# Performance work log

Measured on AMD Instinct MI355X. Metric: run time of the kernel, lower is better.

Reference implementation:

```python
import jax, jax.numpy as jnp
import numpy as np
import math

NUM_HIDDEN = 512

def setup_inputs() -> dict:
    key = jax.random.key(0)
    k1, k2 = jax.random.split(key)
    a = jax.random.normal(k1, (8, 2048, NUM_HIDDEN), dtype=jnp.float32)
    b = jax.random.normal(k2, (8, 2048, NUM_HIDDEN), dtype=jnp.float32)
    return {"a": a, "b": b}

def reference(a, b):
    # simi_matrix: [B, La, Lb] = a @ b^T / sqrt(H)
    scale = 1.0 / math.sqrt(NUM_HIDDEN)
    simi = jnp.einsum('bld,bmd->blm', a, b) * scale
    norm_weight = jax.nn.softmax(simi, axis=2)
    # up_1: [B, La, H] = attn @ b + residual a
    up_1 = jnp.einsum('blm,bmd->bld', norm_weight, b) + a
    return up_1
```

## Files before the change

kernel.cpp:

```cpp
#include <hip/hip_runtime.h>
#include <hip/hip_bf16.h>

#define D 512
#define NSEQ 2048
#define NB 8
#define QBLK 64
#define KVBLK 64
#define NTHREADS 512
#define NT (NSEQ / KVBLK)
#define ROWE 2112
#define BUFE (16 * ROWE)
#define SROWP 68
#define PROWP 72
#define CROWP 68
#define DEFER_THR 8.0f

typedef __attribute__((ext_vector_type(8))) short bf16x8;
typedef __attribute__((ext_vector_type(4))) float f32x4;
typedef __attribute__((ext_vector_type(4))) unsigned short u16x4;
typedef __attribute__((ext_vector_type(4))) int i32x4;

static __device__ __forceinline__ unsigned short f2b(float f) {
  unsigned u = __builtin_bit_cast(unsigned, f);
  return (unsigned short)((u + 0x7FFFu + ((u >> 16) & 1u)) >> 16);
}

__global__ __launch_bounds__(256) void conv_dual(const float* __restrict__ in,
                                                 unsigned short* __restrict__ b16,
                                                 unsigned short* __restrict__ bT) {
  __shared__ unsigned short tile[64 * CROWP];
  const int bid = blockIdx.x;
  const int batch = bid >> 8;
  const int rem = bid & 255;
  const int kvt = rem >> 3;
  const int dt  = rem & 7;
  const int t = threadIdx.x;
  const int r = t >> 2;
  const int c = (t & 3) * 16;

  const float* src = in + ((size_t)batch * NSEQ + kvt * 64 + r) * D + dt * 64 + c;
  unsigned short* o16 = b16 + ((size_t)batch * NSEQ + kvt * 64 + r) * D + dt * 64 + c;

  float4 v0 = *reinterpret_cast<const float4*>(src);
  float4 v1 = *reinterpret_cast<const float4*>(src + 4);
  float4 v2 = *reinterpret_cast<const float4*>(src + 8);
  float4 v3 = *reinterpret_cast<const float4*>(src + 12);
  bf16x8 h0, h1;
  h0[0] = (short)f2b(v0.x); h0[1] = (short)f2b(v0.y);
  h0[2] = (short)f2b(v0.z); h0[3] = (short)f2b(v0.w);
  h0[4] = (short)f2b(v1.x); h0[5] = (short)f2b(v1.y);
  h0[6] = (short)f2b(v1.z); h0[7] = (short)f2b(v1.w);
  h1[0] = (short)f2b(v2.x); h1[1] = (short)f2b(v2.y);
  h1[2] = (short)f2b(v2.z); h1[3] = (short)f2b(v2.w);
  h1[4] = (short)f2b(v3.x); h1[5] = (short)f2b(v3.y);
  h1[6] = (short)f2b(v3.z); h1[7] = (short)f2b(v3.w);
  *reinterpret_cast<bf16x8*>(o16)     = h0;
  *reinterpret_cast<bf16x8*>(o16 + 8) = h1;
  #pragma unroll
  for (int i = 0; i < 4; ++i) {
    u16x4 w;
    w[0] = (unsigned short)((i < 2 ? h0 : h1)[(i & 1) * 4 + 0]);
    w[1] = (unsigned short)((i < 2 ? h0 : h1)[(i & 1) * 4 + 1]);
    w[2] = (unsigned short)((i < 2 ? h0 : h1)[(i & 1) * 4 + 2]);
    w[3] = (unsigned short)((i < 2 ? h0 : h1)[(i & 1) * 4 + 3]);
    *reinterpret_cast<u16x4*>(&tile[r * CROWP + c + i * 4]) = w;
  }
  __syncthreads();

  const int w  = t >> 6;
  const int dr = t & 63;
  unsigned short* oT = bT + (size_t)batch * D * NSEQ
                          + (size_t)(dt * 64 + dr) * NSEQ + kvt * 64 + w * 16;
  unsigned short g[16];
  #pragma unroll
  for (int i = 0; i < 16; ++i)
    g[i] = tile[(w * 16 + i) * CROWP + dr];
  bf16x8 p0, p1;
  #pragma unroll
  for (int i = 0; i < 8; ++i) { p0[i] = (short)g[i]; p1[i] = (short)g[8 + i]; }
  *reinterpret_cast<bf16x8*>(oT)     = p0;
  *reinterpret_cast<bf16x8*>(oT + 8) = p1;
}

__global__ __launch_bounds__(NTHREADS, 1)
void attn_v17(const float* __restrict__ A, const unsigned short* __restrict__ B16,
              const unsigned short* __restrict__ T16, float* __restrict__ Out) {
  __shared__ __align__(16) unsigned short Bs[BUFE];
  __shared__ __align__(16) unsigned short Bt[D * KVBLK];
  __shared__ __align__(16) float Ss[QBLK * SROWP];
  __shared__ __align__(16) unsigned short Ps[QBLK * PROWP];
  __shared__ float mS[QBLK];
  __shared__ float lS[QBLK];
  __shared__ float aS[QBLK];
  __shared__ __align__(16) int flagS[8];

  const int tid  = threadIdx.x;
  const int wid  = tid >> 6;
  const int lane = tid & 63;
  const int l16  = lane & 15;
  const int g4   = lane >> 4;

  const int batch = blockIdx.x & 7;
  const int qt    = blockIdx.x >> 3;
  const int qbase = qt * QBLK;

  const float*          Ab = A   + (size_t)batch * NSEQ * D;
  const unsigned short* Kb = B16 + (size_t)batch * NSEQ * D;
  const unsigned short* Tb = T16 + (size_t)batch * D * NSEQ;
  float*                Ob = Out + (size_t)batch * NSEQ * D;

  const float scale = 0.04419417382415922f;

  const int qi = wid >> 1;
  const int kp = wid & 1;

  const float* Arow = Ab + (size_t)(qbase + qi * 16 + l16) * D;
  bf16x8 qf[16];
  #pragma unroll
  for (int ks = 0; ks < 16; ++ks) {
    int d0 = ks * 32 + g4 * 8;
    float4 v0 = *reinterpret_cast<const float4*>(Arow + d0);
    float4 v1 = *reinterpret_cast<const float4*>(Arow + d0 + 4);
    bf16x8 f;
    f[0] = (short)f2b(v0.x * scale); f[1] = (short)f2b(v0.y * scale);
    f[2] = (short)f2b(v0.z * scale); f[3] = (short)f2b(v0.w * scale);
    f[4] = (short)f2b(v1.x * scale); f[5] = (short)f2b(v1.y * scale);
    f[6] = (short)f2b(v1.z * scale); f[7] = (short)f2b(v1.w * scale);
    qf[ks] = f;
  }
  if (tid < QBLK) { mS[tid] = -1e30f; lS[tid] = 0.f; }

  f32x4 acc[4][4];
  #pragma unroll
  for (int mi = 0; mi < 4; ++mi)
    #pragma unroll
    for (int ni = 0; ni < 4; ++ni)
      acc[mi][ni] = (f32x4){0.f, 0.f, 0.f, 0.f};

  #pragma unroll
  for (int c = 0; c < 8; ++c) {
    int id = wid * 8 + c;
    int g = id >> 2, q = id & 3;
    const unsigned short* src = Kb
        + (size_t)(g * 4 + ((lane >> 1) & 3)) * D
        + q * 128 + (lane >> 3) * 16 + (lane & 1) * 8;
    unsigned short* dst = &Bs[g * ROWE + q * 512];
    __builtin_amdgcn_global_load_lds(
        (const __attribute__((address_space(1))) void*)src,
        (__attribute__((address_space(3))) void*)dst, 16, 0, 0);
  }
  #pragma unroll
  for (int c = 0; c < 8; ++c) {
    int drow = wid * 64 + c * 8 + (lane >> 3);
    int chunk = (lane & 7) ^ ((lane >> 3) & 7);
    const unsigned short* src = Tb + (size_t)drow * NSEQ + chunk * 8;
    unsigned short* dst = (unsigned short*)&Bt[(wid * 64 + c * 8) * KVBLK];
    __builtin_amdgcn_global_load_lds(
        (const __attribute__((address_space(1))) void*)src,
        (__attribute__((address_space(3))) void*)dst, 16, 0, 0);
  }
  asm volatile("s_waitcnt vmcnt(0)" ::: "memory");
  asm volatile("s_waitcnt lgkmcnt(0)" ::: "memory");
  __builtin_amdgcn_s_barrier();

  const int bbase0 = ((kp * 2) * 4 + (l16 >> 2)) * ROWE + (l16 & 3) * 16 + (g4 & 1) * 8;
  const int bbase1 = bbase0 + 4 * ROWE;

  for (int kt = 0; kt < NT; ++kt) {
    {
      f32x4 s0 = {0.f, 0.f, 0.f, 0.f};
      f32x4 s1 = {0.f, 0.f, 0.f, 0.f};
      __builtin_amdgcn_s_setprio(1);
      #pragma unroll
      for (int ks = 0; ks < 16; ++ks) {
        const int ro = (ks * 2 + (g4 >> 1)) * 64;
        const bf16x8 b0 = *reinterpret_cast<const bf16x8*>(&Bs[bbase0 + ro]);
        const bf16x8 b1 = *reinterpret_cast<const bf16x8*>(&Bs[bbase1 + ro]);
        s0 = __builtin_amdgcn_mfma_f32_16x16x32_bf16(qf[ks], b0, s0, 0, 0, 0);
        s1 = __builtin_amdgcn_mfma_f32_16x16x32_bf16(qf[ks], b1, s1, 0, 0, 0);
      }
      __builtin_amdgcn_s_setprio(0);
      #pragma unroll
      for (int r = 0; r < 4; ++r) {
        Ss[(qi * 16 + g4 * 4 + r) * SROWP + (kp * 2) * 16 + l16]     = s0[r];
        Ss[(qi * 16 + g4 * 4 + r) * SROWP + (kp * 2 + 1) * 16 + l16] = s1[r];
      }
    }
    asm volatile("s_waitcnt lgkmcnt(0)" ::: "memory");
    __builtin_amdgcn_s_barrier();

    if (kt + 1 < NT) {
      const unsigned short* Kt = Kb + (size_t)(kt + 1) * KVBLK * D;
      #pragma unroll
      for (int c = 0; c < 8; ++c) {
        int id = wid * 8 + c;
        int g = id >> 2, q = id & 3;
        const unsigned short* src = Kt
            + (size_t)(g * 4 + ((lane >> 1) & 3)) * D
            + q * 128 + (lane >> 3) * 16 + (lane & 1) * 8;
        unsigned short* dst = &Bs[g * ROWE + q * 512];
        __builtin_amdgcn_global_load_lds(
            (const __attribute__((address_space(1))) void*)src,
            (__attribute__((address_space(3))) void*)dst, 16, 0, 0);
      }
    }

    {
      int row = wid * 8 + (lane >> 3);
      int c   = lane & 7;
      float sv[8];
      #pragma unroll
      for (int j = 0; j < 8; ++j)
        sv[j] = Ss[row * SROWP + c + 8 * j];
      float m01 = fmaxf(sv[0], sv[1]), m23 = fmaxf(sv[2], sv[3]);
      float m45 = fmaxf(sv[4], sv[5]), m67 = fmaxf(sv[6], sv[7]);
      float mloc = fmaxf(fmaxf(m01, m23), fmaxf(m45, m67));
      #pragma unroll
      for (int off = 1; off < 8; off <<= 1)
        mloc = fmaxf(mloc, __shfl_xor(mloc, off));
      float mold = mS[row];
      int defer = (mloc <= mold + DEFER_THR) ? 1 : 0;
      float mnew = defer ? mold : mloc;
      float al = defer ? 1.0f : __expf(mold - mnew);
      float psum = 0.f;
      #pragma unroll
      for (int j = 0; j < 8; ++j) {
        float p = __expf(sv[j] - mnew);
        psum += p;
        Ps[row * PROWP + c + 8 * j] = f2b(p);
      }
      #pragma unroll
      for (int off = 1; off < 8; off <<= 1)
        psum += __shfl_xor(psum, off);
      int wave_defer = __all(defer);
      if (c == 0) {
        mS[row] = mnew;
        lS[row] = lS[row] * al + psum;
        aS[row] = al;
      }
      if (lane == 0) flagS[wid] = wave_defer;
    }
    asm volatile("s_waitcnt lgkmcnt(0)" ::: "memory");
    if (kt + 1 < NT) {
      asm volatile("s_waitcnt vmcnt(8)" ::: "memory");
    } else {
      asm volatile("s_waitcnt vmcnt(0)" ::: "memory");
    }
    __builtin_amdgcn_s_barrier();

    {
      i32x4 f0 = *reinterpret_cast<const i32x4*>(&flagS[0]);
      i32x4 f1 = *reinterpret_cast<const i32x4*>(&flagS[4]);
      int allskip = f0[0] & f0[1] & f0[2] & f0[3] & f1[0] & f1[1] & f1[2] & f1[3];
      if (!allskip) {
        #pragma unroll
        for (int mi = 0; mi < 4; ++mi) {
          float a = aS[mi * 16 + l16];
          #pragma unroll
          for (int ni = 0; ni < 4; ++ni)
            #pragma unroll
            for (int r = 0; r < 4; ++r)
              acc[mi][ni][r] *= a;
        }
      }

      const char* Bc = (const char*)&Bt[0];
      __builtin_amdgcn_s_setprio(1);
      #pragma unroll
      for (int ks = 0; ks < 2; ++ks) {
        bf16x8 pf[4];
        #pragma unroll
        for (int mi = 0; mi < 4; ++mi)
          pf[mi] = *reinterpret_cast<const bf16x8*>(
              &Ps[(mi * 16 + l16) * PROWP + ks * 32 + g4 * 8]);
        #pragma unroll
        for (int ni = 0; ni < 4; ++ni) {
          int row = wid * 64 + ni * 16 + l16;
          int swz = (ks * 4 + g4) ^ (l16 & 7);
          const bf16x8 vf = *reinterpret_cast<const bf16x8*>(Bc + row * 128 + swz * 16);
          #pragma unroll
          for (int mi = 0; mi < 4; ++mi)
            acc[mi][ni] = __builtin_amdgcn_mfma_f32_16x16x32_bf16(vf, pf[mi], acc[mi][ni], 0, 0, 0);
        }
      }
      __builtin_amdgcn_s_setprio(0);
    }
    asm volatile("s_waitcnt lgkmcnt(0)" ::: "memory");

    if (kt + 1 < NT) {
      #pragma unroll
      for (int c = 0; c < 8; ++c) {
        int drow = wid * 64 + c * 8 + (lane >> 3);
        int chunk = (lane & 7) ^ ((lane >> 3) & 7);
        const unsigned short* src = Tb + (size_t)drow * NSEQ + (kt + 1) * KVBLK + chunk * 8;
        unsigned short* dst = (unsigned short*)&Bt[(wid * 64 + c * 8) * KVBLK];
        __builtin_amdgcn_global_load_lds(
            (const __attribute__((address_space(1))) void*)src,
            (__attribute__((address_space(3))) void*)dst, 16, 0, 0);
      }
      asm volatile("s_waitcnt vmcnt(8)" ::: "memory");
    }
    __builtin_amdgcn_s_barrier();
  }

  #pragma unroll
  for (int mi = 0; mi < 4; ++mi) {
    float rl = 1.0f / lS[mi * 16 + l16];
    int q = qbase + mi * 16 + l16;
    #pragma unroll
    for (int ni = 0; ni < 4; ++ni) {
      int d = wid * 64 + ni * 16 + g4 * 4;
      const float4 av = *reinterpret_cast<const float4*>(Ab + (size_t)q * D + d);
      float4 o;
      o.x = acc[mi][ni][0] * rl + av.x;
      o.y = acc[mi][ni][1] * rl + av.y;
      o.z = acc[mi][ni][2] * rl + av.z;
      o.w = acc[mi][ni][3] * rl + av.w;
      *reinterpret_cast<float4*>(Ob + (size_t)q * D + d) = o;
    }
  }
}

#define FQBLK 32
#define FSROWP (64 + 4)
#define FPROWP (64 + 8)
__global__ __launch_bounds__(NTHREADS, 2)
void attn_fb(const float* __restrict__ A, const float* __restrict__ B32,
             float* __restrict__ Out) {
  __shared__ __align__(16) unsigned short Bs[BUFE];
  __shared__ float Ss[FQBLK * FSROWP];
  __shared__ unsigned short Ps[FQBLK * FPROWP];
  __shared__ float mS[FQBLK];
  __shared__ float lS[FQBLK];
  __shared__ float aS[FQBLK];

  const int tid  = threadIdx.x;
  const int wid  = tid >> 6;
  const int lane = tid & 63;
  const int l16  = lane & 15;
  const int g4   = lane >> 4;

  const int batch = blockIdx.x & 7;
  const int qt    = blockIdx.x >> 3;
  const int qbase = qt * FQBLK;

  const float* Ab   = A   + (size_t)batch * NSEQ * D;
  const float* Bb32 = B32 + (size_t)batch * NSEQ * D;
  float*       Ob   = Out + (size_t)batch * NSEQ * D;

  const float scale = 0.04419417382415922f;

  const int qi = wid >> 2;
  const int ki = wid & 3;

  const float* Arow = Ab + (size_t)(qbase + qi * 16 + l16) * D;
  bf16x8 qf[16];
  #pragma unroll
  for (int ks = 0; ks < 16; ++ks) {
    int d0 = ks * 32 + g4 * 8;
    float4 v0 = *reinterpret_cast<const float4*>(Arow + d0);
    float4 v1 = *reinterpret_cast<const float4*>(Arow + d0 + 4);
    bf16x8 f;
    f[0] = (short)f2b(v0.x * scale); f[1] = (short)f2b(v0.y * scale);
    f[2] = (short)f2b(v0.z * scale); f[3] = (short)f2b(v0.w * scale);
    f[4] = (short)f2b(v1.x * scale); f[5] = (short)f2b(v1.y * scale);
    f[6] = (short)f2b(v1.z * scale); f[7] = (short)f2b(v1.w * scale);
    qf[ks] = f;
  }
  if (tid < FQBLK) { mS[tid] = -1e30f; lS[tid] = 0.f; }

  f32x4 acc[2][4];
  #pragma unroll
  for (int mi = 0; mi < 2; ++mi)
    #pragma unroll
    for (int ni = 0; ni < 4; ++ni)
      acc[mi][ni] = (f32x4){0.f, 0.f, 0.f, 0.f};

  for (int kt = 0; kt < NT; ++kt) {
    __builtin_amdgcn_s_barrier();
    const float* Bt2 = Bb32 + (size_t)kt * KVBLK * D;
    #pragma unroll
    for (int c = 0; c < 8; ++c) {
      int id = wid * 8 + c;
      int g = id >> 2, q = id & 3;
      int kv = g * 4 + ((lane >> 1) & 3);
      int d  = q * 128 + (lane >> 3) * 16 + (lane & 1) * 8;
      const float* s = Bt2 + (size_t)kv * D + d;
      float4 v0 = *reinterpret_cast<const float4*>(s);
      float4 v1 = *reinterpret_cast<const float4*>(s + 4);
      bf16x8 h;
      h[0] = (short)f2b(v0.x); h[1] = (short)f2b(v0.y);
      h[2] = (short)f2b(v0.z); h[3] = (short)f2b(v0.w);
      h[4] = (short)f2b(v1.x); h[5] = (short)f2b(v1.y);
      h[6] = (short)f2b(v1.z); h[7] = (short)f2b(v1.w);
      *reinterpret_cast<bf16x8*>(&Bs[g * ROWE + q * 512 + lane * 8]) = h;
    }
    asm volatile("s_waitcnt lgkmcnt(0)" ::: "memory");
    __builtin_amdgcn_s_barrier();

    {
      f32x4 s = {0.f, 0.f, 0.f, 0.f};
      const int bbase = (ki * 4 + (l16 >> 2)) * ROWE + (l16 & 3) * 16 + (g4 & 1) * 8;
      #pragma unroll
      for (int ks = 0; ks < 16; ++ks) {
        const bf16x8 bf = *reinterpret_cast<const bf16x8*>(
            &Bs[bbase + (ks * 2 + (g4 >> 1)) * 64]);
        s = __builtin_amdgcn_mfma_f32_16x16x32_bf16(qf[ks], bf, s, 0, 0, 0);
      }
      #pragma unroll
      for (int r = 0; r < 4; ++r)
        Ss[(qi * 16 + g4 * 4 + r) * FSROWP + ki * 16 + l16] = s[r];
    }
    asm volatile("s_waitcnt lgkmcnt(0)" ::: "memory");
    __builtin_amdgcn_s_barrier();

    {
      int row = wid * 4 + g4;
      float sv[4];
      float mloc = -1e30f;
      #pragma unroll
      for (int j = 0; j < 4; ++j) {
        sv[j] = Ss[row * FSROWP + l16 + 16 * j];
        mloc = fmaxf(mloc, sv[j]);
      }
      #pragma unroll
      for (int off = 1; off < 16; off <<= 1)
        mloc = fmaxf(mloc, __shfl_xor(mloc, off));
      float mold = mS[row];
      float mnew = fmaxf(mold, mloc);
      float al = __expf(mold - mnew);
      float psum = 0.f;
      #pragma unroll
      for (int j = 0; j < 4; ++j) {
        float p = __expf(sv[j] - mnew);
        psum += p;
        Ps[row * FPROWP + l16 + 16 * j] = f2b(p);
      }
      #pragma unroll
      for (int off = 1; off < 16; off <<= 1)
        psum += __shfl_xor(psum, off);
      if (l16 == 0) {
        mS[row] = mnew;
        lS[row] = lS[row] * al + psum;
        aS[row] = al;
      }
    }
    asm volatile("s_waitcnt lgkmcnt(0)" ::: "memory");
    __builtin_amdgcn_s_barrier();

    {
      #pragma unroll
      for (int mi = 0; mi < 2; ++mi)
        #pragma unroll
        for (int r = 0; r < 4; ++r) {
          float a = aS[mi * 16 + g4 * 4 + r];
          #pragma unroll
          for (int ni = 0; ni < 4; ++ni)
            acc[mi][ni][r] *= a;
        }

      #pragma unroll
      for (int ks = 0; ks < 2; ++ks) {
        bf16x8 pf[2];
        #pragma unroll
        for (int mi = 0; mi < 2; ++mi)
          pf[mi] = *reinterpret_cast<const bf16x8*>(
              &Ps[(mi * 16 + l16) * FPROWP + ks * 32 + g4 * 8]);
        #pragma unroll
        for (int ni = 0; ni < 4; ++ni) {
          bf16x8 vv;
          #pragma unroll
          for (int j = 0; j < 8; ++j)
            vv[j] = (short)Bs[(ks * 8 + g4 * 2 + (j >> 2)) * ROWE
                              + (wid * 4 + ni) * 64 + (j & 3) * 16 + l16];
          #pragma unroll
          for (int mi = 0; mi < 2; ++mi)
            acc[mi][ni] = __builtin_amdgcn_mfma_f32_16x16x32_bf16(pf[mi], vv, acc[mi][ni], 0, 0, 0);
        }
      }
    }
  }

  #pragma unroll
  for (int mi = 0; mi < 2; ++mi)
    #pragma unroll
    for (int r = 0; r < 4; ++r) {
      float rl = 1.0f / lS[mi * 16 + g4 * 4 + r];
      #pragma unroll
      for (int ni = 0; ni < 4; ++ni) {
        int q = qbase + mi * 16 + g4 * 4 + r;
        int d = wid * 64 + ni * 16 + l16;
        size_t off = (size_t)q * D + d;
        Ob[off] = acc[mi][ni][r] * rl + Ab[off];
      }
    }
}

extern "C" void kernel_launch(void* const* d_in, const int* in_sizes, int n_in,
                              void* d_out, int out_size, void* d_ws, size_t ws_size,
                              hipStream_t stream) {
  const float* a = (const float*)d_in[0];
  const float* b = (const float*)d_in[1];
  float* out = (float*)d_out;
  const size_t one = (size_t)NB * NSEQ * D * sizeof(unsigned short);
  dim3 block(NTHREADS);
  if (ws_size >= 2 * one) {
    unsigned short* b16 = (unsigned short*)d_ws;
    unsigned short* bT  = b16 + (size_t)NB * NSEQ * D;
    conv_dual<<<NB * 256, 256, 0, stream>>>(b, b16, bT);
    dim3 grid(NB * (NSEQ / QBLK));
    attn_v17<<<grid, block, 0, stream>>>(a, b16, bT, out);
  } else {
    dim3 grid(NB * (NSEQ / FQBLK));
    attn_fb<<<grid, block, 0, stream>>>(a, b, out);
  }
}
```

Baseline: 132.6 us.

## Compute softmax directly from MFMA registers instead of staging scores in LDS

The QK^T MFMA operands are swapped so each lane holds one query row's scores. Row max and sum can then be reduced in registers, with a small LDS exchange between the two key-half waves. This removes the fp32 score buffer in shared memory along with its store/load round trip, and writes P as bf16 directly from registers. In exchange it adds a cross-wave max exchange and a deferred row-sum update after the second barrier, and it shrinks LDS use.

```diff
diff --git a/kernel.cpp b/kernel.cpp
--- a/kernel.cpp
+++ b/kernel.cpp
@@ -10,7 +10,6 @@
 #define NT (NSEQ / KVBLK)
 #define ROWE 2112
 #define BUFE (16 * ROWE)
-#define SROWP 68
 #define PROWP 72
 #define CROWP 68
 #define DEFER_THR 8.0f
@@ -83,15 +82,16 @@
 }
 
 __global__ __launch_bounds__(NTHREADS, 1)
-void attn_v17(const float* __restrict__ A, const unsigned short* __restrict__ B16,
+void attn_v18(const float* __restrict__ A, const unsigned short* __restrict__ B16,
               const unsigned short* __restrict__ T16, float* __restrict__ Out) {
   __shared__ __align__(16) unsigned short Bs[BUFE];
   __shared__ __align__(16) unsigned short Bt[D * KVBLK];
-  __shared__ __align__(16) float Ss[QBLK * SROWP];
   __shared__ __align__(16) unsigned short Ps[QBLK * PROWP];
   __shared__ float mS[QBLK];
   __shared__ float lS[QBLK];
   __shared__ float aS[QBLK];
+  __shared__ float pmaxS[128];
+  __shared__ float psumS[128];
   __shared__ __align__(16) int flagS[8];
 
   const int tid  = threadIdx.x;
@@ -167,86 +167,93 @@
   const int bbase1 = bbase0 + 4 * ROWE;
 
   for (int kt = 0; kt < NT; ++kt) {
+    f32x4 s0 = {0.f, 0.f, 0.f, 0.f};
+    f32x4 s1 = {0.f, 0.f, 0.f, 0.f};
+    __builtin_amdgcn_s_setprio(1);
+    #pragma unroll
+    for (int ks = 0; ks < 16; ++ks) {
+      const int ro = (ks * 2 + (g4 >> 1)) * 64;
+      const bf16x8 b0 = *reinterpret_cast<const bf16x8*>(&Bs[bbase0 + ro]);
+      const bf16x8 b1 = *reinterpret_cast<const bf16x8*>(&Bs[bbase1 + ro]);
+      s0 = __builtin_amdgcn_mfma_f32_16x16x32_bf16(b0, qf[ks], s0, 0, 0, 0);
+      s1 = __builtin_amdgcn_mfma_f32_16x16x32_bf16(b1, qf[ks], s1, 0, 0, 0);
+    }
+    __builtin_amdgcn_s_setprio(0);
+
     {
-      f32x4 s0 = {0.f, 0.f, 0.f, 0.f};
-      f32x4 s1 = {0.f, 0.f, 0.f, 0.f};
-      __builtin_amdgcn_s_setprio(1);
-      #pragma unroll
-      for (int ks = 0; ks < 16; ++ks) {
-        const int ro = (ks * 2 + (g4 >> 1)) * 64;
-        const bf16x8 b0 = *reinterpret_cast<const bf16x8*>(&Bs[bbase0 + ro]);
-        const bf16x8 b1 = *reinterpret_cast<const bf16x8*>(&Bs[bbase1 + ro]);
-        s0 = __builtin_amdgcn_mfma_f32_16x16x32_bf16(qf[ks], b0, s0, 0, 0, 0);
-        s1 = __builtin_amdgcn_mfma_f32_16x16x32_bf16(qf[ks], b1, s1, 0, 0, 0);
-      }
-      __builtin_amdgcn_s_setprio(0);
+      float m01 = fmaxf(s0[0], s0[1]), m23 = fmaxf(s0[2], s0[3]);
+      float m45 = fmaxf(s1[0], s1[1]), m67 = fmaxf(s1[2], s1[3]);
+      float mloc = fmaxf(fmaxf(m01, m23), fmaxf(m45, m67));
+      mloc = fmaxf(mloc, __shfl_xor(mloc, 16));
+      mloc = fmaxf(mloc, __shfl_xor(mloc, 32));
+      if (lane < 16) pmaxS[qi * 32 + kp * 16 + lane] = mloc;
+      asm volatile("s_waitcnt lgkmcnt(0)" ::: "memory");
+      __builtin_amdgcn_s_barrier();
+
+      if (kt + 1 < NT) {
+        const unsigned short* Kt = Kb + (size_t)(kt + 1) * KVBLK * D;
+        #pragma unroll
+        for (int c = 0; c < 8; ++c) {
+          int id = wid * 8 + c;
+          int g = id >> 2, q = id & 3;
+          const unsigned short* src = Kt
+              + (size_t)(g * 4 + ((lane >> 1) & 3)) * D
+              + q * 128 + (lane >> 3) * 16 + (lane & 1) * 8;
+          unsigned short* dst = &Bs[g * ROWE + q * 512];
+          __builtin_amdgcn_global_load_lds(
+              (const __attribute__((address_space(1))) void*)src,
+              (__attribute__((address_space(3))) void*)dst, 16, 0, 0);
+        }
+      }
+
+      float mpart = pmaxS[qi * 32 + (kp ^ 1) * 16 + l16];
+      float mcomb = fmaxf(mloc, mpart);
+      float mold = mS[qi * 16 + l16];
+      int defer = (mcomb <= mold + DEFER_THR) ? 1 : 0;
+      float mnew = defer ? mold : mcomb;
+      float al = defer ? 1.0f : __expf(mold - mnew);
+
+      float rowsum = 0.f;
+      u16x4 w0, w1;
       #pragma unroll
       for (int r = 0; r < 4; ++r) {
-        Ss[(qi * 16 + g4 * 4 + r) * SROWP + (kp * 2) * 16 + l16]     = s0[r];
-        Ss[(qi * 16 + g4 * 4 + r) * SROWP + (kp * 2 + 1) * 16 + l16] = s1[r];
-      }
-    }
-    asm volatile("s_waitcnt lgkmcnt(0)" ::: "memory");
-    __builtin_amdgcn_s_barrier();
-
-    if (kt + 1 < NT) {
-      const unsigned short* Kt = Kb + (size_t)(kt + 1) * KVBLK * D;
-      #pragma unroll
-      for (int c = 0; c < 8; ++c) {
-        int id = wid * 8 + c;
-        int g = id >> 2, q = id & 3;
-        const unsigned short* src = Kt
-            + (size_t)(g * 4 + ((lane >> 1) & 3)) * D
-            + q * 128 + (lane >> 3) * 16 + (lane & 1) * 8;
-        unsigned short* dst = &Bs[g * ROWE + q * 512];
-        __builtin_amdgcn_global_load_lds(
-            (const __attribute__((address_space(1))) void*)src,
-            (__attribute__((address_space(3))) void*)dst, 16, 0, 0);
-      }
-    }
-
-    {
-      int row = wid * 8 + (lane >> 3);
-      int c   = lane & 7;
-      float sv[8];
-      #pragma unroll
-      for (int j = 0; j < 8; ++j)
-        sv[j] = Ss[row * SROWP + c + 8 * j];
-      float m01 = fmaxf(sv[0], sv[1]), m23 = fmaxf(sv[2], sv[3]);
-      float m45 = fmaxf(sv[4], sv[5]), m67 = fmaxf(sv[6], sv[7]);
-      float mloc = fmaxf(fmaxf(m01, m23), fmaxf(m45, m67));
-      #pragma unroll
-      for (int off = 1; off < 8; off <<= 1)
-        mloc = fmaxf(mloc, __shfl_xor(mloc, off));
-      float mold = mS[row];
-      int defer = (mloc <= mold + DEFER_THR) ? 1 : 0;
-      float mnew = defer ? mold : mloc;
-      float al = defer ? 1.0f : __expf(mold - mnew);
-      float psum = 0.f;
-      #pragma unroll
-      for (int j = 0; j < 8; ++j) {
-        float p = __expf(sv[j] - mnew);
-        psum += p;
-        Ps[row * PROWP + c + 8 * j] = f2b(p);
-      }
-      #pragma unroll
-      for (int off = 1; off < 8; off <<= 1)
-        psum += __shfl_xor(psum, off);
+        float p = __expf(s0[r] - mnew);
+        rowsum += p;
+        w0[r] = f2b(p);
+      }
+      #pragma unroll
+      for (int r = 0; r < 4; ++r) {
+        float p = __expf(s1[r] - mnew);
+        rowsum += p;
+        w1[r] = f2b(p);
+      }
+      const int prow = (qi * 16 + l16) * PROWP + 32 * kp + 4 * g4;
+      *reinterpret_cast<u16x4*>(&Ps[prow])      = w0;
+      *reinterpret_cast<u16x4*>(&Ps[prow + 16]) = w1;
+
+      rowsum += __shfl_xor(rowsum, 16);
+      rowsum += __shfl_xor(rowsum, 32);
+      if (lane < 16) psumS[qi * 32 + kp * 16 + lane] = rowsum;
       int wave_defer = __all(defer);
-      if (c == 0) {
-        mS[row] = mnew;
-        lS[row] = lS[row] * al + psum;
-        aS[row] = al;
+      if (kp == 0 && lane < 16) {
+        mS[qi * 16 + lane] = mnew;
+        aS[qi * 16 + lane] = al;
       }
       if (lane == 0) flagS[wid] = wave_defer;
-    }
-    asm volatile("s_waitcnt lgkmcnt(0)" ::: "memory");
-    if (kt + 1 < NT) {
-      asm volatile("s_waitcnt vmcnt(8)" ::: "memory");
-    } else {
-      asm volatile("s_waitcnt vmcnt(0)" ::: "memory");
-    }
-    __builtin_amdgcn_s_barrier();
+
+      asm volatile("s_waitcnt lgkmcnt(0)" ::: "memory");
+      if (kt + 1 < NT) {
+        asm volatile("s_waitcnt vmcnt(8)" ::: "memory");
+      } else {
+        asm volatile("s_waitcnt vmcnt(0)" ::: "memory");
+      }
+      __builtin_amdgcn_s_barrier();
+
+      if (kp == 0 && lane < 16) {
+        float pp = psumS[qi * 32 + 16 + lane];
+        lS[qi * 16 + lane] = lS[qi * 16 + lane] * al + rowsum + pp;
+      }
+    }
 
     {
       i32x4 f0 = *reinterpret_cast<const i32x4*>(&flagS[0]);
@@ -509,7 +516,7 @@
     unsigned short* bT  = b16 + (size_t)NB * NSEQ * D;
     conv_dual<<<NB * 256, 256, 0, stream>>>(b, b16, bT);
     dim3 grid(NB * (NSEQ / QBLK));
-    attn_v17<<<grid, block, 0, stream>>>(a, b16, bT, out);
+    attn_v18<<<grid, block, 0, stream>>>(a, b16, bT, out);
   } else {
     dim3 grid(NB * (NSEQ / FQBLK));
     attn_fb<<<grid, block, 0, stream>>>(a, b, out);
```

Result: no change. 131.1 us, median of 2 (-1.1%).
